# Performance work log

Measured on AMD Instinct MI355X. Metric: run time of the kernel, lower is better.

The kernel has to match this reference:

```python
import jax, jax.numpy as jnp
import numpy as np

C = 256; G = 8; GC = C // G; K = 3; PAD = 1; DIL = 1; STRIDE = 1
P = K * K
BN_EPS = 1e-5; LN_EPS = 1e-5


def setup_inputs() -> dict:
    key = jax.random.key(0)
    ks = jax.random.split(key, 8)
    def rn(k, shape, scale=0.02):
        return jax.random.normal(k, shape, jnp.float32) * scale
    B, H, W = 8, 56, 56
    return dict(
        x=jax.random.normal(ks[0], (B, C, H, W), jnp.float32),
        w_in=rn(ks[1], (C, C)), b_in=jnp.zeros((C,), jnp.float32),
        dw_w=rn(ks[2], (C, 1, K, K)), dw_b=jnp.zeros((C,), jnp.float32),
        ln_g=jnp.ones((C,), jnp.float32), ln_b=jnp.zeros((C,), jnp.float32),
        w_off=rn(ks[3], (C, G * P * 2)), b_off=jnp.zeros((G * P * 2,), jnp.float32),
        w_mask=rn(ks[4], (C, G * P)), b_mask=jnp.zeros((G * P,), jnp.float32),
        w_out=rn(ks[5], (C, C)), b_out=jnp.zeros((C,), jnp.float32),
        bn_g=jnp.ones((C,), jnp.float32), bn_b=jnp.zeros((C,), jnp.float32),
        bn_mean=jnp.zeros((C,), jnp.float32),
        bn_var=jnp.ones((C,), jnp.float32),
    )


def _forward(x, w_in, b_in, dw_w, dw_b, ln_g, ln_b, w_off, b_off,
             w_mask, b_mask, w_out, b_out, bn_g, bn_b, bn_mean, bn_var):
    B, _, H, W = x.shape
    x_nhwc = jnp.transpose(x, (0, 2, 3, 1))                    # [B,H,W,C]
    v = x_nhwc @ w_in + b_in                                   # input_proj

    # offset/mask branch: depthwise conv (NCHW) + LayerNorm (channels_last) + GELU
    f = jax.lax.conv_general_dilated(
        x, dw_w, (1, 1), [(PAD, PAD), (PAD, PAD)],
        feature_group_count=C,
        dimension_numbers=('NCHW', 'OIHW', 'NCHW')) + dw_b[None, :, None, None]
    f = jnp.transpose(f, (0, 2, 3, 1))                         # [B,H,W,C]
    mu = f.mean(-1, keepdims=True)
    var = f.var(-1, keepdims=True)
    f = (f - mu) * jax.lax.rsqrt(var + LN_EPS) * ln_g + ln_b
    f = jax.nn.gelu(f, approximate=False)

    offset = (f @ w_off + b_off).reshape(B, H, W, G, P, 2)     # (x, y) pairs
    mask = jax.nn.softmax((f @ w_mask + b_mask).reshape(B, H, W, G, P), axis=-1)

    # zero-pad projected features (dcnv3_core_pytorch pads before sampling)
    vp = jnp.pad(v, ((0, 0), (PAD, PAD), (PAD, PAD), (0, 0)))
    Hin, Win = H + 2 * PAD, W + 2 * PAD

    # reference points + kernel dilation grid, normalized to padded extent
    base = (DIL * (K - 1)) // 2 + 0.5
    ref_y = (base + jnp.arange(H, dtype=jnp.float32) * STRIDE) / Hin   # [H]
    ref_x = (base + jnp.arange(W, dtype=jnp.float32) * STRIDE) / Win   # [W]
    kx = jnp.arange(K, dtype=jnp.float32) * DIL - (DIL * (K - 1)) // 2
    gx, gy = jnp.meshgrid(kx, kx, indexing='ij')               # torch meshgrid order
    grid_x = gx.reshape(-1) / Win                              # [P]
    grid_y = gy.reshape(-1) / Hin

    loc_x = ref_x[None, None, :, None, None] + grid_x[None, None, None, None, :] + offset[..., 0] / Win
    loc_y = ref_y[None, :, None, None, None] + grid_y[None, None, None, None, :] + offset[..., 1] / Hin
    # grid_sample(align_corners=False) pixel coords: p = loc * size - 0.5
    px = loc_x * Win - 0.5                                     # [B,H,W,G,P]
    py = loc_y * Hin - 0.5

    x0 = jnp.floor(px); y0 = jnp.floor(py)
    wx = px - x0; wy = py - y0
    x0i = x0.astype(jnp.int32); y0i = y0.astype(jnp.int32)
    x1i = x0i + 1; y1i = y0i + 1

    def valid(i, lim):
        return ((i >= 0) & (i < lim)).astype(v.dtype)
    vx0, vx1 = valid(x0i, Win), valid(x1i, Win)
    vy0, vy1 = valid(y0i, Hin), valid(y1i, Hin)
    x0c = jnp.clip(x0i, 0, Win - 1); x1c = jnp.clip(x1i, 0, Win - 1)
    y0c = jnp.clip(y0i, 0, Hin - 1); y1c = jnp.clip(y1i, 0, Hin - 1)

    vg = vp.reshape(B, Hin * Win, G, GC).transpose(0, 2, 1, 3).reshape(B * G, Hin * Win, GC)
    L = H * W

    def regroup(a):  # [B,H,W,G,P] -> [B*G, L*P]
        return a.reshape(B, L, G, P).transpose(0, 2, 1, 3).reshape(B * G, L * P)

    def gather(yc, xc):
        idx = regroup(yc * Win + xc)
        return jnp.take_along_axis(vg, idx[:, :, None], axis=1)   # [B*G, L*P, GC]

    sampled = (gather(y0c, x0c) * regroup((1 - wx) * (1 - wy) * vx0 * vy0)[:, :, None]
             + gather(y0c, x1c) * regroup(wx * (1 - wy) * vx1 * vy0)[:, :, None]
             + gather(y1c, x0c) * regroup((1 - wx) * wy * vx0 * vy1)[:, :, None]
             + gather(y1c, x1c) * regroup(wx * wy * vx1 * vy1)[:, :, None])

    m = mask.reshape(B, L, G, P).transpose(0, 2, 1, 3)             # [B,G,L,P]
    out = (sampled.reshape(B, G, L, P, GC) * m[..., None]).sum(3)  # [B,G,L,GC]
    out = out.transpose(0, 2, 1, 3).reshape(B, H, W, C)

    out = out @ w_out + b_out                                  # output_proj
    y = jnp.transpose(out, (0, 3, 1, 2))                       # NCHW
    y = (y - bn_mean[None, :, None, None]) * jax.lax.rsqrt(bn_var + BN_EPS)[None, :, None, None] \
        * bn_g[None, :, None, None] + bn_b[None, :, None, None]
    return y * jax.nn.sigmoid(y)                               # SiLU


def reference(x, w_in, b_in, dw_w, dw_b, ln_g, ln_b, w_off, b_off,
              w_mask, b_mask, w_out, b_out, bn_g, bn_b, bn_mean, bn_var):
    return _forward(x, w_in, b_in, dw_w, dw_b, ln_g, ln_b, w_off, b_off,
                    w_mask, b_mask, w_out, b_out, bn_g, bn_b, bn_mean, bn_var)
```

## Files before the change

kernel.cpp:

```cpp
#include <hip/hip_runtime.h>
#include <math.h>

#define BATCH 8
#define CH    256
#define HDIM  56
#define WDIM  56
#define HW    (HDIM*WDIM)
#define MTOT  (BATCH*HW)
#define GRP   8
#define GC    32
#define NP    9
#define NOFF  (GRP*NP*2)
#define NMSK  (GRP*NP)
#define NTOT  (NOFF+NMSK)
#define POSB  4
#define DWBLK (MTOT/POSB)
#define XTBLK (49*4*8)
#define NBLKG ((MTOT/64)*2)

typedef float f32x4 __attribute__((ext_vector_type(4)));
typedef short s16x8 __attribute__((ext_vector_type(8)));

__device__ inline void split2(float a, float b, unsigned int& hp, unsigned int& lp)
{
    const unsigned int ua = __float_as_uint(a), ub = __float_as_uint(b);
    hp = (ub & 0xffff0000u) | (ua >> 16);
    const float ha = __uint_as_float(ua & 0xffff0000u);
    const float hb = __uint_as_float(ub & 0xffff0000u);
    const unsigned int la = __float_as_uint(a - ha), lb = __float_as_uint(b - hb);
    lp = (lb & 0xffff0000u) | (la >> 16);
}

__device__ __forceinline__ void gld_lds16(const unsigned short* g, unsigned short* l)
{
    __builtin_amdgcn_global_load_lds(
        (const __attribute__((address_space(1))) unsigned int*)g,
        (__attribute__((address_space(3))) unsigned int*)l, 16, 0, 0);
}

__device__ __forceinline__ void gemm64x128_body(
    const unsigned short* __restrict__ ahi,
    const unsigned short* __restrict__ alo,
    const unsigned short* __restrict__ whi,
    const unsigned short* __restrict__ wlo,
    unsigned short* sAh, unsigned short* sAl,
    unsigned short* sBh, unsigned short* sBl,
    int m0, int n0g, int t, f32x4 (&acc)[4][2])
{
    const int lane = t & 63, wv4 = t >> 6;
    const int wm = wv4 >> 1;
    const int wn = wv4 & 1;
    const int fm = lane & 15, q = lane >> 4;

    const int arow0 = t >> 2;
    const int asl0  = (t & 3) ^ ((arow0 >> 1) & 3);
    const int albase0 = wv4 * 512;
    int brow[2], bsl[2], blbase[2];
    #pragma unroll
    for (int i = 0; i < 2; ++i) {
        const int u = i * 256 + t;
        brow[i] = u >> 2;
        bsl[i] = (u & 3) ^ ((brow[i] >> 1) & 3);
        blbase[i] = i * 2048 + wv4 * 512;
    }

    for (int kk = 0; kk < 8; ++kk) {
        const int k0 = kk * 32;
        {
            const size_t ga = (size_t)(m0 + arow0) * CH + k0 + asl0 * 8;
            gld_lds16(ahi + ga, sAh + albase0);
            gld_lds16(alo + ga, sAl + albase0);
        }
        #pragma unroll
        for (int i = 0; i < 2; ++i) {
            const size_t gb = (size_t)(n0g + brow[i]) * CH + k0 + bsl[i] * 8;
            gld_lds16(whi + gb, sBh + blbase[i]);
            gld_lds16(wlo + gb, sBl + blbase[i]);
        }
        __syncthreads();

        s16x8 ah[2], al[2], wh[4], wl[4];
        #pragma unroll
        for (int i = 0; i < 2; ++i) {
            const int ar = wm * 32 + i * 16 + fm;
            const int as = (q ^ ((ar >> 1) & 3)) * 8;
            ah[i] = *(const s16x8*)&sAh[ar * 32 + as];
            al[i] = *(const s16x8*)&sAl[ar * 32 + as];
        }
        #pragma unroll
        for (int i = 0; i < 4; ++i) {
            const int br = wn * 64 + i * 16 + fm;
            const int bs = (q ^ ((br >> 1) & 3)) * 8;
            wh[i] = *(const s16x8*)&sBh[br * 32 + bs];
            wl[i] = *(const s16x8*)&sBl[br * 32 + bs];
        }
        #pragma unroll
        for (int nt = 0; nt < 4; ++nt)
            #pragma unroll
            for (int mt = 0; mt < 2; ++mt) {
                acc[nt][mt] = __builtin_amdgcn_mfma_f32_16x16x32_bf16(wh[nt], ah[mt], acc[nt][mt], 0, 0, 0);
                acc[nt][mt] = __builtin_amdgcn_mfma_f32_16x16x32_bf16(wh[nt], al[mt], acc[nt][mt], 0, 0, 0);
                acc[nt][mt] = __builtin_amdgcn_mfma_f32_16x16x32_bf16(wl[nt], ah[mt], acc[nt][mt], 0, 0, 0);
            }
        __syncthreads();
    }
}

__device__ __forceinline__ void dw_body(
    const unsigned short* __restrict__ xhi,
    const unsigned short* __restrict__ xlo,
    const float* __restrict__ dw_w,
    const float* __restrict__ dw_b,
    const float* __restrict__ ln_g,
    const float* __restrict__ ln_b,
    unsigned short* __restrict__ fh,
    unsigned short* __restrict__ fl,
    float* wt, float* lbias, float* lgam, float* lbet,
    int bid, int t)
{
    {
        const float* wp = dw_w + t * NP;
        #pragma unroll
        for (int p = 0; p < NP; ++p) wt[p * CH + t] = wp[p];
        lbias[t] = dw_b[t]; lgam[t] = ln_g[t]; lbet[t] = ln_b[t];
    }
    __syncthreads();

    const int per = DWBLK / 8;
    const int sw  = (bid & 7) * per + (bid >> 3);
    const int q   = t >> 6, lane = t & 63;
    const int n   = sw * POSB + q;
    const int b   = n / HW;
    const int hw  = n % HW;
    const int h   = hw / WDIM, w = hw % WDIM;
    const int c4  = lane * 4;
    const size_t base = (size_t)b * HW * CH + c4;

    float ax = 0.0f, ay = 0.0f, az = 0.0f, aw = 0.0f;
    #pragma unroll
    for (int p = 0; p < NP; ++p) {
        const int hh = h + p / 3 - 1;
        const int ww = w + p % 3 - 1;
        if ((unsigned)hh >= (unsigned)HDIM || (unsigned)ww >= (unsigned)WDIM)
            continue;
        const size_t idx = base + (size_t)(hh * WDIM + ww) * CH;
        const ushort4 uh = *(const ushort4*)(xhi + idx);
        const ushort4 ul = *(const ushort4*)(xlo + idx);
        const float4 wv = *(const float4*)&wt[p * CH + c4];
        ax = fmaf(__uint_as_float((unsigned)uh.x << 16), wv.x,
             fmaf(__uint_as_float((unsigned)ul.x << 16), wv.x, ax));
        ay = fmaf(__uint_as_float((unsigned)uh.y << 16), wv.y,
             fmaf(__uint_as_float((unsigned)ul.y << 16), wv.y, ay));
        az = fmaf(__uint_as_float((unsigned)uh.z << 16), wv.z,
             fmaf(__uint_as_float((unsigned)ul.z << 16), wv.z, az));
        aw = fmaf(__uint_as_float((unsigned)uh.w << 16), wv.w,
             fmaf(__uint_as_float((unsigned)ul.w << 16), wv.w, aw));
    }
    {
        const float4 b4 = *(const float4*)&lbias[c4];
        ax += b4.x; ay += b4.y; az += b4.z; aw += b4.w;
    }

    float s1 = ax + ay + az + aw;
    float s2 = ax*ax + ay*ay + az*az + aw*aw;
    #pragma unroll
    for (int off = 32; off > 0; off >>= 1) {
        s1 += __shfl_xor(s1, off);
        s2 += __shfl_xor(s2, off);
    }
    const float mean = s1 * (1.0f / 256.0f);
    const float rstd = rsqrtf(s2 * (1.0f / 256.0f) - mean * mean + 1e-5f);

    const float4 g4 = *(const float4*)&lgam[c4];
    const float4 e4 = *(const float4*)&lbet[c4];
    const float x0 = (ax - mean) * rstd * g4.x + e4.x;
    const float x1 = (ay - mean) * rstd * g4.y + e4.y;
    const float x2 = (az - mean) * rstd * g4.z + e4.z;
    const float x3 = (aw - mean) * rstd * g4.w + e4.w;
    const float o0 = 0.5f * x0 * (1.0f + erff(x0 * 0.70710678118654752f));
    const float o1 = 0.5f * x1 * (1.0f + erff(x1 * 0.70710678118654752f));
    const float o2 = 0.5f * x2 * (1.0f + erff(x2 * 0.70710678118654752f));
    const float o3 = 0.5f * x3 * (1.0f + erff(x3 * 0.70710678118654752f));

    unsigned int hp0, lp0, hp1, lp1;
    split2(o0, o1, hp0, lp0);
    split2(o2, o3, hp1, lp1);
    *(uint2*)&fh[(size_t)n * CH + c4] = make_uint2(hp0, hp1);
    *(uint2*)&fl[(size_t)n * CH + c4] = make_uint2(lp0, lp1);
}

__global__ __launch_bounds__(256)
void prep_kernel(const float* __restrict__ x,
                 unsigned short* __restrict__ xt_hi,
                 unsigned short* __restrict__ xt_lo,
                 const float* __restrict__ w_out,
                 unsigned short* __restrict__ wt_hi,
                 unsigned short* __restrict__ wt_lo,
                 const float* __restrict__ w_in,
                 unsigned short* __restrict__ wt3_hi,
                 unsigned short* __restrict__ wt3_lo,
                 const float* __restrict__ w_off,
                 const float* __restrict__ w_mask,
                 const float* __restrict__ b_off,
                 const float* __restrict__ b_mask,
                 unsigned short* __restrict__ wt2_hi,
                 unsigned short* __restrict__ wt2_lo,
                 float* __restrict__ bcat)
{
    __shared__ float lds[64][68];
    const int bid = blockIdx.x;
    const int t = threadIdx.x;

    if (bid < XTBLK) {
        const int hw0 = (bid % 49) * 64;
        const int k0  = ((bid / 49) % 4) * 64;
        const int b   = bid / 196;
        #pragma unroll
        for (int p = 0; p < 4; ++p) {
            const int kr = (t >> 4) + p * 16;
            const int hc = (t & 15) * 4;
            *(float4*)&lds[kr][hc] =
                *(const float4*)(x + ((size_t)b * CH + k0 + kr) * HW + hw0 + hc);
        }
        __syncthreads();
        const int ml = t >> 2;
        const int kc = (t & 3) * 16;
        unsigned int hbuf[8], lbuf[8];
        #pragma unroll
        for (int j = 0; j < 16; j += 2)
            split2(lds[kc + j][ml], lds[kc + j + 1][ml], hbuf[j >> 1], lbuf[j >> 1]);
        const size_t row = (size_t)(b * HW + hw0 + ml) * CH + k0 + kc;
        *(uint4*)&xt_hi[row]     = *(uint4*)&hbuf[0];
        *(uint4*)&xt_hi[row + 8] = *(uint4*)&hbuf[4];
        *(uint4*)&xt_lo[row]     = *(uint4*)&lbuf[0];
        *(uint4*)&xt_lo[row + 8] = *(uint4*)&lbuf[4];
    } else if (bid < XTBLK + 32) {
        const int u = bid - XTBLK;
        const float* w = (u < 16) ? w_out : w_in;
        unsigned short* hi = (u < 16) ? wt_hi : wt3_hi;
        unsigned short* lo = (u < 16) ? wt_lo : wt3_lo;
        const int uu = u & 15;
        const int kt = (uu & 3) * 64, nt = (uu >> 2) * 64;
        #pragma unroll
        for (int p = 0; p < 4; ++p) {
            const int kr = (t >> 4) + p * 16, nc = (t & 15) * 4;
            *(float4*)&lds[kr][nc] = *(const float4*)(w + (size_t)(kt + kr) * CH + nt + nc);
        }
        __syncthreads();
        const int nl = t >> 2, kc = (t & 3) * 16;
        #pragma unroll
        for (int j = 0; j < 16; j += 2) {
            const float f0 = lds[kc + j][nl], f1 = lds[kc + j + 1][nl];
            unsigned int hp, lp;
            split2(f0, f1, hp, lp);
            *(unsigned int*)&hi[(size_t)(nt + nl) * CH + kt + kc + j] = hp;
            *(unsigned int*)&lo[(size_t)(nt + nl) * CH + kt + kc + j] = lp;
        }
    } else {
        const int u = bid - XTBLK - 32;
        const int n = t;
        if (u == 0) {
            bcat[n] = (n < NOFF) ? b_off[n] : ((n < NTOT) ? b_mask[n - NOFF] : 0.0f);
        }
        const int k0 = u * 16;
        #pragma unroll
        for (int j = 0; j < 16; j += 2) {
            const int k = k0 + j;
            float f0 = 0.0f, f1 = 0.0f;
            if (n < NOFF) {
                f0 = w_off[(size_t)k * NOFF + n];
                f1 = w_off[(size_t)(k + 1) * NOFF + n];
            } else if (n < NTOT) {
                f0 = w_mask[(size_t)k * NMSK + (n - NOFF)];
                f1 = w_mask[(size_t)(k + 1) * NMSK + (n - NOFF)];
            }
            unsigned int hp, lp;
            split2(f0, f1, hp, lp);
            *(unsigned int*)&wt2_hi[(size_t)n * CH + k] = hp;
            *(unsigned int*)&wt2_lo[(size_t)n * CH + k] = lp;
        }
    }
}

__global__ __launch_bounds__(256)
void dw_and_gemm_v(const unsigned short* __restrict__ xhi,
                   const unsigned short* __restrict__ xlo,
                   const float* __restrict__ dw_w,
                   const float* __restrict__ dw_b,
                   const float* __restrict__ ln_g,
                   const float* __restrict__ ln_b,
                   unsigned short* __restrict__ fh,
                   unsigned short* __restrict__ fl,
                   const unsigned short* __restrict__ whi,
                   const unsigned short* __restrict__ wlo,
                   const float* __restrict__ bias,
                   float* __restrict__ v)
{
    __shared__ alignas(16) char smem[24576];
    const int bid = blockIdx.x;
    const int t = threadIdx.x;

    if (bid < DWBLK) {
        float* wt    = (float*)smem;
        float* lbias = (float*)(smem + NP * CH * 4);
        float* lgam  = lbias + CH;
        float* lbet  = lgam + CH;
        dw_body(xhi, xlo, dw_w, dw_b, ln_g, ln_b, fh, fl,
                wt, lbias, lgam, lbet, bid, t);
    } else {
        unsigned short* sAh = (unsigned short*)smem;
        unsigned short* sAl = sAh + 64 * 32;
        unsigned short* sBh = sAl + 64 * 32;
        unsigned short* sBl = sBh + 128 * 32;
        const int lbid = bid - DWBLK;
        const int sw = (lbid & 7) * (NBLKG / 8) + (lbid >> 3);
        const int m0  = (sw >> 1) * 64;
        const int n0g = (sw & 1) * 128;
        const int lane = t & 63, wv4 = t >> 6;
        const int wm = wv4 >> 1, wn = wv4 & 1;
        const int fm = lane & 15, q = lane >> 4;

        f32x4 acc[4][2];
        const f32x4 zero = {0.0f, 0.0f, 0.0f, 0.0f};
        #pragma unroll
        for (int i = 0; i < 4; ++i)
            #pragma unroll
            for (int j = 0; j < 2; ++j) acc[i][j] = zero;

        gemm64x128_body(xhi, xlo, whi, wlo, sAh, sAl, sBh, sBl, m0, n0g, t, acc);

        #pragma unroll
        for (int nt = 0; nt < 4; ++nt) {
            const int n = n0g + wn*64 + nt*16 + q*4;
            const float4 b4 = *(const float4*)&bias[n];
            #pragma unroll
            for (int mt = 0; mt < 2; ++mt) {
                const int mm = m0 + wm*32 + mt*16 + fm;
                f32x4 o = acc[nt][mt];
                o[0] += b4.x; o[1] += b4.y; o[2] += b4.z; o[3] += b4.w;
                *(f32x4*)&v[(size_t)mm * CH + n] = o;
            }
        }
    }
}

__global__ __launch_bounds__(256)
void gemm_omb(const unsigned short* __restrict__ ahi,
              const unsigned short* __restrict__ alo,
              const unsigned short* __restrict__ whi,
              const unsigned short* __restrict__ wlo,
              const float* __restrict__ bias,
              float* __restrict__ omb)
{
    __shared__ unsigned short sAh[64*32], sAl[64*32], sBh[128*32], sBl[128*32];

    const int sw = (blockIdx.x & 7) * (NBLKG / 8) + (blockIdx.x >> 3);
    const int m0  = (sw >> 1) * 64;
    const int n0g = (sw & 1) * 128;
    const int t = threadIdx.x;
    const int lane = t & 63, wv4 = t >> 6;
    const int wm = wv4 >> 1, wn = wv4 & 1;
    const int fm = lane & 15, q = lane >> 4;

    f32x4 acc[4][2];
    const f32x4 zero = {0.0f, 0.0f, 0.0f, 0.0f};
    #pragma unroll
    for (int i = 0; i < 4; ++i)
        #pragma unroll
        for (int j = 0; j < 2; ++j) acc[i][j] = zero;

    gemm64x128_body(ahi, alo, whi, wlo, sAh, sAl, sBh, sBl, m0, n0g, t, acc);

    #pragma unroll
    for (int nt = 0; nt < 4; ++nt) {
        const int n = n0g + wn*64 + nt*16 + q*4;
        const float4 b4 = *(const float4*)&bias[n];
        #pragma unroll
        for (int mt = 0; mt < 2; ++mt) {
            const int mm = m0 + wm*32 + mt*16 + fm;
            f32x4 o = acc[nt][mt];
            o[0] += b4.x; o[1] += b4.y; o[2] += b4.z; o[3] += b4.w;
            *(f32x4*)&omb[(size_t)mm * CH + n] = o;
        }
    }
}

__global__ __launch_bounds__(256)
void gemm_out_64x128(const unsigned short* __restrict__ ahi,
                     const unsigned short* __restrict__ alo,
                     const unsigned short* __restrict__ whi,
                     const unsigned short* __restrict__ wlo,
                     const float* __restrict__ bias,
                     const float* __restrict__ bn_g,
                     const float* __restrict__ bn_b,
                     const float* __restrict__ bn_mean,
                     const float* __restrict__ bn_var,
                     float* __restrict__ y)
{
    __shared__ unsigned short sAh[64*32], sAl[64*32], sBh[128*32], sBl[128*32];

    const int sw = (blockIdx.x & 7) * (NBLKG / 8) + (blockIdx.x >> 3);
    const int m0  = (sw >> 1) * 64;
    const int n0g = (sw & 1) * 128;
    const int t = threadIdx.x;
    const int lane = t & 63, wv4 = t >> 6;
    const int wm = wv4 >> 1, wn = wv4 & 1;
    const int fm = lane & 15, q = lane >> 4;

    f32x4 acc[4][2];
    const f32x4 zero = {0.0f, 0.0f, 0.0f, 0.0f};
    #pragma unroll
    for (int i = 0; i < 4; ++i)
        #pragma unroll
        for (int j = 0; j < 2; ++j) acc[i][j] = zero;

    gemm64x128_body(ahi, alo, whi, wlo, sAh, sAl, sBh, sBl, m0, n0g, t, acc);

    #pragma unroll
    for (int nt = 0; nt < 4; ++nt) {
        #pragma unroll
        for (int r = 0; r < 4; ++r) {
            const int n = n0g + wn*64 + nt*16 + q*4 + r;
            const float sc = bn_g[n] * rsqrtf(bn_var[n] + 1e-5f);
            const float sb = bn_b[n] - bn_mean[n] * sc;
            const float bs = bias[n];
            #pragma unroll
            for (int mt = 0; mt < 2; ++mt) {
                const int mm = m0 + wm*32 + mt*16 + fm;
                const int bimg = mm / HW, hw = mm % HW;
                float val = (acc[nt][mt][r] + bs) * sc + sb;
                y[(size_t)bimg * CH * HW + (size_t)n * HW + hw] = val / (1.0f + expf(-val));
            }
        }
    }
}

__global__ __launch_bounds__(256)
void sample_kernel_omb_split(const float* __restrict__ v,
                             const float* __restrict__ omb,
                             unsigned short* __restrict__ sh,
                             unsigned short* __restrict__ sl)
{
    __shared__ alignas(16) float loff[POSB][NOFF];
    __shared__ alignas(16) float lmsk[POSB][NMSK];
    __shared__ alignas(16) float wtab[POSB][GRP*NP][4];
    __shared__ alignas(16) int   itab[POSB][GRP*NP][4];

    const int per  = DWBLK / 8;
    const int bid  = blockIdx.x;
    const int sw   = (bid % 8) * per + (bid / 8);
    const int n0 = sw * POSB;
    const int t = threadIdx.x;

    if (t < POSB * (NOFF/4)) {
        const int q = t / (NOFF/4), r = t % (NOFF/4);
        *(float4*)&loff[q][r*4] = *(const float4*)&omb[(size_t)(n0+q)*CH + r*4];
    } else if (t < POSB * (NOFF/4) + POSB * (NMSK/4)) {
        const int u = t - POSB * (NOFF/4);
        const int q = u / (NMSK/4), r = u % (NMSK/4);
        *(float4*)&lmsk[q][r*4] = *(const float4*)&omb[(size_t)(n0+q)*CH + NOFF + r*4];
    }
    __syncthreads();

    if (t < POSB * GRP) {
        const int q = t >> 3, g = t & 7;
        float* mm = &lmsk[q][g * NP];
        float mx = -1e30f;
        #pragma unroll
        for (int p = 0; p < NP; ++p) mx = fmaxf(mx, mm[p]);
        float sum = 0.0f;
        #pragma unroll
        for (int p = 0; p < NP; ++p) { const float e = __expf(mm[p] - mx); mm[p] = e; sum += e; }
        const float inv = 1.0f / sum;
        #pragma unroll
        for (int p = 0; p < NP; ++p) mm[p] *= inv;
    }
    __syncthreads();

    for (int u = t; u < POSB * GRP * NP; u += 256) {
        const int q = u / (GRP*NP), j = u % (GRP*NP);
        const int g = j / NP, p = j % NP;
        const int n = n0 + q;
        const int hw = n % HW;
        const int h = hw / WDIM, w = hw % WDIM;
        const float ox = loff[q][g*18 + p*2 + 0];
        const float oy = loff[q][g*18 + p*2 + 1];
        const float m  = lmsk[q][g*NP + p];
        const float px = (float)(w + p/3) + ox;
        const float py = (float)(h + p%3) + oy;
        const float fx = floorf(px), fy = floorf(py);
        const float wx = px - fx, wy = py - fy;
        const int x0 = (int)fx, y0 = (int)fy;
        const int x1 = x0 + 1, y1 = y0 + 1;
        const float vx0 = (x0 >= 1 && x0 < 57) ? 1.0f : 0.0f;
        const float vx1 = (x1 >= 1 && x1 < 57) ? 1.0f : 0.0f;
        const float vy0 = (y0 >= 1 && y0 < 57) ? 1.0f : 0.0f;
        const float vy1 = (y1 >= 1 && y1 < 57) ? 1.0f : 0.0f;
        const int x0c = min(max(x0, 1), 56), x1c = min(max(x1, 1), 56);
        const int y0c = min(max(y0, 1), 56), y1c = min(max(y1, 1), 56);
        wtab[q][j][0] = m * (1.0f-wx) * (1.0f-wy) * vx0 * vy0;
        wtab[q][j][1] = m * wx        * (1.0f-wy) * vx1 * vy0;
        wtab[q][j][2] = m * (1.0f-wx) * wy        * vx0 * vy1;
        wtab[q][j][3] = m * wx        * wy        * vx1 * vy1;
        itab[q][j][0] = ((y0c-1)*WDIM + (x0c-1)) * CH;
        itab[q][j][1] = ((y0c-1)*WDIM + (x1c-1)) * CH;
        itab[q][j][2] = ((y1c-1)*WDIM + (x0c-1)) * CH;
        itab[q][j][3] = ((y1c-1)*WDIM + (x1c-1)) * CH;
    }
    __syncthreads();

    const int q = t >> 6, lane = t & 63;
    const int n = n0 + q;
    const int b = n / HW;
    const int g = lane >> 3;
    const float* vb = v + (size_t)b*HW*CH + lane*4;
    float4 acc = {0.0f, 0.0f, 0.0f, 0.0f};
    #pragma unroll
    for (int p = 0; p < NP; ++p) {
        const int j = g*NP + p;
        const float4 wv = *(const float4*)&wtab[q][j][0];
        const int4  iv = *(const int4*)&itab[q][j][0];
        const float4 c0 = *(const float4*)(vb + iv.x);
        const float4 c1 = *(const float4*)(vb + iv.y);
        const float4 c2 = *(const float4*)(vb + iv.z);
        const float4 c3 = *(const float4*)(vb + iv.w);
        acc.x += wv.x*c0.x + wv.y*c1.x + wv.z*c2.x + wv.w*c3.x;
        acc.y += wv.x*c0.y + wv.y*c1.y + wv.z*c2.y + wv.w*c3.y;
        acc.z += wv.x*c0.z + wv.y*c1.z + wv.z*c2.z + wv.w*c3.z;
        acc.w += wv.x*c0.w + wv.y*c1.w + wv.z*c2.w + wv.w*c3.w;
    }
    unsigned int hp0, lp0, hp1, lp1;
    split2(acc.x, acc.y, hp0, lp0);
    split2(acc.z, acc.w, hp1, lp1);
    *(uint2*)&sh[(size_t)n*CH + lane*4] = make_uint2(hp0, hp1);
    *(uint2*)&sl[(size_t)n*CH + lane*4] = make_uint2(lp0, lp1);
}

__global__ __launch_bounds__(256)
void xt_split_kernel(const float* __restrict__ x,
                     unsigned short* __restrict__ hi,
                     unsigned short* __restrict__ lo)
{
    __shared__ float lds[64][68];
    const int hw0 = blockIdx.x * 64;
    const int k0  = blockIdx.y * 64;
    const int b   = blockIdx.z;
    const int t = threadIdx.x;
    #pragma unroll
    for (int p = 0; p < 4; ++p) {
        const int kr = (t >> 4) + p * 16;
        const int hc = (t & 15) * 4;
        *(float4*)&lds[kr][hc] =
            *(const float4*)(x + ((size_t)b * CH + k0 + kr) * HW + hw0 + hc);
    }
    __syncthreads();
    const int ml = t >> 2;
    const int kc = (t & 3) * 16;
    unsigned int hbuf[8], lbuf[8];
    #pragma unroll
    for (int j = 0; j < 16; j += 2)
        split2(lds[kc + j][ml], lds[kc + j + 1][ml], hbuf[j >> 1], lbuf[j >> 1]);
    const size_t row = (size_t)(b * HW + hw0 + ml) * CH + k0 + kc;
    *(uint4*)&hi[row]     = *(uint4*)&hbuf[0];
    *(uint4*)&hi[row + 8] = *(uint4*)&hbuf[4];
    *(uint4*)&lo[row]     = *(uint4*)&lbuf[0];
    *(uint4*)&lo[row + 8] = *(uint4*)&lbuf[4];
}

__global__ __launch_bounds__(256)
void wt_split_kernel(const float* __restrict__ w,
                     unsigned short* __restrict__ hi,
                     unsigned short* __restrict__ lo)
{
    __shared__ float lds[64][68];
    const int kt = blockIdx.x * 64, nt = blockIdx.y * 64;
    const int t = threadIdx.x;
    #pragma unroll
    for (int p = 0; p < 4; ++p) {
        const int kr = (t >> 4) + p * 16, nc = (t & 15) * 4;
        *(float4*)&lds[kr][nc] = *(const float4*)(w + (size_t)(kt + kr) * CH + nt + nc);
    }
    __syncthreads();
    const int nl = t >> 2, kc = (t & 3) * 16;
    #pragma unroll
    for (int j = 0; j < 16; j += 2) {
        const float f0 = lds[kc + j][nl], f1 = lds[kc + j + 1][nl];
        unsigned int hp, lp;
        split2(f0, f1, hp, lp);
        *(unsigned int*)&hi[(size_t)(nt + nl) * CH + kt + kc + j] = hp;
        *(unsigned int*)&lo[(size_t)(nt + nl) * CH + kt + kc + j] = lp;
    }
}

__global__ __launch_bounds__(256)
void wt2_split_kernel(const float* __restrict__ w_off,
                      const float* __restrict__ w_mask,
                      const float* __restrict__ b_off,
                      const float* __restrict__ b_mask,
                      unsigned short* __restrict__ hi,
                      unsigned short* __restrict__ lo,
                      float* __restrict__ bcat)
{
    const int n = threadIdx.x;
    if (blockIdx.x == 0) {
        bcat[n] = (n < NOFF) ? b_off[n] : ((n < NTOT) ? b_mask[n - NOFF] : 0.0f);
    }
    const int k0 = blockIdx.x * 16;
    #pragma unroll
    for (int j = 0; j < 16; j += 2) {
        const int k = k0 + j;
        float f0 = 0.0f, f1 = 0.0f;
        if (n < NOFF) {
            f0 = w_off[(size_t)k * NOFF + n];
            f1 = w_off[(size_t)(k + 1) * NOFF + n];
        } else if (n < NTOT) {
            f0 = w_mask[(size_t)k * NMSK + (n - NOFF)];
            f1 = w_mask[(size_t)(k + 1) * NMSK + (n - NOFF)];
        }
        unsigned int hp, lp;
        split2(f0, f1, hp, lp);
        *(unsigned int*)&hi[(size_t)n * CH + k] = hp;
        *(unsigned int*)&lo[(size_t)n * CH + k] = lp;
    }
}

__global__ __launch_bounds__(256)
void gemm_in_mfma(const unsigned short* __restrict__ xhi,
                  const unsigned short* __restrict__ xlo,
                  const unsigned short* __restrict__ whi,
                  const unsigned short* __restrict__ wlo,
                  const float* __restrict__ bias,
                  float* __restrict__ v)
{
    const int m0 = blockIdx.x * 256;
    const int n0 = blockIdx.y * 64;
    const int t = threadIdx.x;
    const int lane = t & 63, wv = t >> 6;
    const int mblk = m0 + wv * 64;
    const int fm = lane & 15;
    const int q  = lane >> 4;

    f32x4 acc[4][4];
    const f32x4 zero = {0.0f, 0.0f, 0.0f, 0.0f};
    #pragma unroll
    for (int i = 0; i < 4; ++i)
        #pragma unroll
        for (int j = 0; j < 4; ++j) acc[i][j] = zero;

    const unsigned short *xrh[4], *xrl[4], *wrh[4], *wrl[4];
    #pragma unroll
    for (int mt = 0; mt < 4; ++mt) {
        xrh[mt] = xhi + (size_t)(mblk + mt*16 + fm) * CH + q * 8;
        xrl[mt] = xlo + (size_t)(mblk + mt*16 + fm) * CH + q * 8;
    }
    #pragma unroll
    for (int nt = 0; nt < 4; ++nt) {
        wrh[nt] = whi + (size_t)(n0 + nt*16 + fm) * CH + q * 8;
        wrl[nt] = wlo + (size_t)(n0 + nt*16 + fm) * CH + q * 8;
    }

    for (int k0 = 0; k0 < CH; k0 += 32) {
        s16x8 wh[4], wl[4], ah[4], al[4];
        #pragma unroll
        for (int nt = 0; nt < 4; ++nt) {
            wh[nt] = *(const s16x8*)(wrh[nt] + k0);
            wl[nt] = *(const s16x8*)(wrl[nt] + k0);
        }
        #pragma unroll
        for (int mt = 0; mt < 4; ++mt) {
            ah[mt] = *(const s16x8*)(xrh[mt] + k0);
            al[mt] = *(const s16x8*)(xrl[mt] + k0);
        }
        #pragma unroll
        for (int nt = 0; nt < 4; ++nt)
            #pragma unroll
            for (int mt = 0; mt < 4; ++mt) {
                acc[nt][mt] = __builtin_amdgcn_mfma_f32_16x16x32_bf16(wh[nt], ah[mt], acc[nt][mt], 0, 0, 0);
                acc[nt][mt] = __builtin_amdgcn_mfma_f32_16x16x32_bf16(wh[nt], al[mt], acc[nt][mt], 0, 0, 0);
                acc[nt][mt] = __builtin_amdgcn_mfma_f32_16x16x32_bf16(wl[nt], ah[mt], acc[nt][mt], 0, 0, 0);
            }
    }

    #pragma unroll
    for (int nt = 0; nt < 4; ++nt) {
        const float4 b4 = *(const float4*)&bias[n0 + nt*16 + q*4];
        #pragma unroll
        for (int mt = 0; mt < 4; ++mt) {
            f32x4 o = acc[nt][mt];
            o[0] += b4.x; o[1] += b4.y; o[2] += b4.z; o[3] += b4.w;
            *(f32x4*)&v[(size_t)(mblk + mt*16 + fm) * CH + n0 + nt*16 + q*4] = o;
        }
    }
}

__global__ __launch_bounds__(256)
void dw_ln_gelu_nhwc_split(const unsigned short* __restrict__ xhi,
                           const unsigned short* __restrict__ xlo,
                           const float* __restrict__ dw_w,
                           const float* __restrict__ dw_b,
                           const float* __restrict__ ln_g,
                           const float* __restrict__ ln_b,
                           unsigned short* __restrict__ fh,
                           unsigned short* __restrict__ fl)
{
    __shared__ float wt[NP][CH];
    __shared__ float lbias[CH], lgam[CH], lbet[CH];
    const int t = threadIdx.x;
    {
        const float* wp = dw_w + t * NP;
        #pragma unroll
        for (int p = 0; p < NP; ++p) wt[p][t] = wp[p];
        lbias[t] = dw_b[t]; lgam[t] = ln_g[t]; lbet[t] = ln_b[t];
    }
    __syncthreads();

    const int per  = DWBLK / 8;
    const int bid  = blockIdx.x;
    const int sw   = (bid & 7) * per + (bid >> 3);
    const int q    = t >> 6, lane = t & 63;
    const int n    = sw * POSB + q;
    const int b    = n / HW;
    const int hw   = n % HW;
    const int h    = hw / WDIM, w = hw % WDIM;
    const int c4   = lane * 4;
    const size_t base = (size_t)b * HW * CH + c4;

    float ax = 0.0f, ay = 0.0f, az = 0.0f, aw = 0.0f;
    #pragma unroll
    for (int p = 0; p < NP; ++p) {
        const int hh = h + p / 3 - 1;
        const int ww = w + p % 3 - 1;
        if ((unsigned)hh >= (unsigned)HDIM || (unsigned)ww >= (unsigned)WDIM)
            continue;
        const size_t idx = base + (size_t)(hh * WDIM + ww) * CH;
        const ushort4 uh = *(const ushort4*)(xhi + idx);
        const ushort4 ul = *(const ushort4*)(xlo + idx);
        const float4 wv = *(const float4*)&wt[p][c4];
        ax = fmaf(__uint_as_float((unsigned)uh.x << 16), wv.x,
             fmaf(__uint_as_float((unsigned)ul.x << 16), wv.x, ax));
        ay = fmaf(__uint_as_float((unsigned)uh.y << 16), wv.y,
             fmaf(__uint_as_float((unsigned)ul.y << 16), wv.y, ay));
        az = fmaf(__uint_as_float((unsigned)uh.z << 16), wv.z,
             fmaf(__uint_as_float((unsigned)ul.z << 16), wv.z, az));
        aw = fmaf(__uint_as_float((unsigned)uh.w << 16), wv.w,
             fmaf(__uint_as_float((unsigned)ul.w << 16), wv.w, aw));
    }
    {
        const float4 b4 = *(const float4*)&lbias[c4];
        ax += b4.x; ay += b4.y; az += b4.z; aw += b4.w;
    }
    float s1 = ax + ay + az + aw;
    float s2 = ax*ax + ay*ay + az*az + aw*aw;
    #pragma unroll
    for (int off = 32; off > 0; off >>= 1) {
        s1 += __shfl_xor(s1, off);
        s2 += __shfl_xor(s2, off);
    }
    const float mean = s1 * (1.0f / 256.0f);
    const float rstd = rsqrtf(s2 * (1.0f / 256.0f) - mean * mean + 1e-5f);
    const float4 g4 = *(const float4*)&lgam[c4];
    const float4 e4 = *(const float4*)&lbet[c4];
    const float x0 = (ax - mean) * rstd * g4.x + e4.x;
    const float x1 = (ay - mean) * rstd * g4.y + e4.y;
    const float x2 = (az - mean) * rstd * g4.z + e4.z;
    const float x3 = (aw - mean) * rstd * g4.w + e4.w;
    const float o0 = 0.5f * x0 * (1.0f + erff(x0 * 0.70710678118654752f));
    const float o1 = 0.5f * x1 * (1.0f + erff(x1 * 0.70710678118654752f));
    const float o2 = 0.5f * x2 * (1.0f + erff(x2 * 0.70710678118654752f));
    const float o3 = 0.5f * x3 * (1.0f + erff(x3 * 0.70710678118654752f));
    unsigned int hp0, lp0, hp1, lp1;
    split2(o0, o1, hp0, lp0);
    split2(o2, o3, hp1, lp1);
    *(uint2*)&fh[(size_t)n * CH + c4] = make_uint2(hp0, hp1);
    *(uint2*)&fl[(size_t)n * CH + c4] = make_uint2(lp0, lp1);
}

__global__ __launch_bounds__(256)
void gemm_out_bf16(const unsigned short* __restrict__ shp,
                   const unsigned short* __restrict__ slp,
                   const unsigned short* __restrict__ whi,
                   const unsigned short* __restrict__ wlo,
                   const float* __restrict__ bias,
                   const float* __restrict__ bn_g,
                   const float* __restrict__ bn_b,
                   const float* __restrict__ bn_mean,
                   const float* __restrict__ bn_var,
                   float* __restrict__ y)
{
    const int m0 = blockIdx.x * 256;
    const int n0 = blockIdx.y * 64;
    const int t = threadIdx.x;
    const int lane = t & 63, wv = t >> 6;
    const int mblk = m0 + wv * 64;
    const int fm = lane & 15;
    const int q  = lane >> 4;

    f32x4 acc[4][4];
    const f32x4 zero = {0.0f, 0.0f, 0.0f, 0.0f};
    #pragma unroll
    for (int i = 0; i < 4; ++i)
        #pragma unroll
        for (int j = 0; j < 4; ++j) acc[i][j] = zero;

    const unsigned short *xrh[4], *xrl[4], *wrh[4], *wrl[4];
    #pragma unroll
    for (int mt = 0; mt < 4; ++mt) {
        xrh[mt] = shp + (size_t)(mblk + mt*16 + fm) * CH + q * 8;
        xrl[mt] = slp + (size_t)(mblk + mt*16 + fm) * CH + q * 8;
    }
    #pragma unroll
    for (int nt = 0; nt < 4; ++nt) {
        wrh[nt] = whi + (size_t)(n0 + nt*16 + fm) * CH + q * 8;
        wrl[nt] = wlo + (size_t)(n0 + nt*16 + fm) * CH + q * 8;
    }

    for (int k0 = 0; k0 < CH; k0 += 32) {
        s16x8 wh[4], wl[4], ah[4], al[4];
        #pragma unroll
        for (int nt = 0; nt < 4; ++nt) {
            wh[nt] = *(const s16x8*)(wrh[nt] + k0);
            wl[nt] = *(const s16x8*)(wrl[nt] + k0);
        }
        #pragma unroll
        for (int mt = 0; mt < 4; ++mt) {
            ah[mt] = *(const s16x8*)(xrh[mt] + k0);
            al[mt] = *(const s16x8*)(xrl[mt] + k0);
        }
        #pragma unroll
        for (int nt = 0; nt < 4; ++nt)
            #pragma unroll
            for (int mt = 0; mt < 4; ++mt) {
                acc[nt][mt] = __builtin_amdgcn_mfma_f32_16x16x32_bf16(wh[nt], ah[mt], acc[nt][mt], 0, 0, 0);
                acc[nt][mt] = __builtin_amdgcn_mfma_f32_16x16x32_bf16(wh[nt], al[mt], acc[nt][mt], 0, 0, 0);
                acc[nt][mt] = __builtin_amdgcn_mfma_f32_16x16x32_bf16(wl[nt], ah[mt], acc[nt][mt], 0, 0, 0);
            }
    }

    #pragma unroll
    for (int nt = 0; nt < 4; ++nt) {
        #pragma unroll
        for (int r = 0; r < 4; ++r) {
            const int n = n0 + nt*16 + q*4 + r;
            const float sc = bn_g[n] * rsqrtf(bn_var[n] + 1e-5f);
            const float sb = bn_b[n] - bn_mean[n] * sc;
            const float bs = bias[n];
            #pragma unroll
            for (int mt = 0; mt < 4; ++mt) {
                const int mm = mblk + mt*16;
                const size_t base = (size_t)(mm / HW) * CH * HW + (mm % HW);
                float val = (acc[nt][mt][r] + bs) * sc + sb;
                y[base + (size_t)n * HW + fm] = val / (1.0f + expf(-val));
            }
        }
    }
}

extern "C" void kernel_launch(void* const* d_in, const int* in_sizes, int n_in,
                              void* d_out, int out_size, void* d_ws, size_t ws_size,
                              hipStream_t stream) {
    const float* x      = (const float*)d_in[0];
    const float* w_in   = (const float*)d_in[1];
    const float* b_in   = (const float*)d_in[2];
    const float* dw_w   = (const float*)d_in[3];
    const float* dw_b   = (const float*)d_in[4];
    const float* ln_g   = (const float*)d_in[5];
    const float* ln_b   = (const float*)d_in[6];
    const float* w_off  = (const float*)d_in[7];
    const float* b_off  = (const float*)d_in[8];
    const float* w_mask = (const float*)d_in[9];
    const float* b_mask = (const float*)d_in[10];
    const float* w_out  = (const float*)d_in[11];
    const float* b_out  = (const float*)d_in[12];
    const float* bn_g   = (const float*)d_in[13];
    const float* bn_b   = (const float*)d_in[14];
    const float* bn_mean= (const float*)d_in[15];
    const float* bn_var = (const float*)d_in[16];
    float* out = (float*)d_out;

    const size_t SZ = (size_t)MTOT * CH;
    const size_t need_new =
        4 * SZ * sizeof(float)
        + 6 * (size_t)CH * CH * sizeof(unsigned short)
        + CH * sizeof(float);

    if (ws_size >= need_new) {
        float* ws = (float*)d_ws;
        float* v    = ws;
        unsigned short* xt_hi = (unsigned short*)(v + SZ);
        unsigned short* xt_lo = xt_hi + SZ;
        unsigned short* fh    = xt_lo + SZ;
        unsigned short* fl    = fh + SZ;
        float* omb  = (float*)(fl + SZ);
        unsigned short* wt_hi  = (unsigned short*)(omb + SZ);
        unsigned short* wt_lo  = wt_hi + CH * CH;
        unsigned short* wt2_hi = wt_lo + CH * CH;
        unsigned short* wt2_lo = wt2_hi + CH * CH;
        unsigned short* wt3_hi = wt2_lo + CH * CH;
        unsigned short* wt3_lo = wt3_hi + CH * CH;
        float* bcat = (float*)(wt3_lo + CH * CH);
        unsigned short* sh = xt_hi;
        unsigned short* sl = xt_lo;

        prep_kernel<<<dim3(XTBLK + 48), dim3(256), 0, stream>>>(
            x, xt_hi, xt_lo, w_out, wt_hi, wt_lo, w_in, wt3_hi, wt3_lo,
            w_off, w_mask, b_off, b_mask, wt2_hi, wt2_lo, bcat);
        dw_and_gemm_v<<<dim3(DWBLK + NBLKG), dim3(256), 0, stream>>>(
            xt_hi, xt_lo, dw_w, dw_b, ln_g, ln_b, fh, fl,
            wt3_hi, wt3_lo, b_in, v);
        gemm_omb<<<dim3(NBLKG), dim3(256), 0, stream>>>(
            fh, fl, wt2_hi, wt2_lo, bcat, omb);
        sample_kernel_omb_split<<<dim3(DWBLK), dim3(256), 0, stream>>>(v, omb, sh, sl);
        gemm_out_64x128<<<dim3(NBLKG), dim3(256), 0, stream>>>(
            sh, sl, wt_hi, wt_lo, b_out, bn_g, bn_b, bn_mean, bn_var, out);
    } else {
        float* ws = (float*)d_ws;
        float* v    = ws;
        unsigned short* xt_hi = (unsigned short*)(v + SZ);
        unsigned short* xt_lo = xt_hi + SZ;
        unsigned short* fh    = xt_lo + SZ;
        unsigned short* fl    = fh + SZ;
        float* omb  = (float*)(fl + SZ);
        unsigned short* wt_hi  = (unsigned short*)(omb + SZ);
        unsigned short* wt_lo  = wt_hi + CH * CH;
        unsigned short* wt2_hi = wt_lo + CH * CH;
        unsigned short* wt2_lo = wt2_hi + CH * CH;
        unsigned short* wt3_hi = wt2_lo + CH * CH;
        unsigned short* wt3_lo = wt3_hi + CH * CH;
        float* bcat = (float*)(wt3_lo + CH * CH);
        unsigned short* sh = xt_hi;
        unsigned short* sl = xt_lo;

        wt_split_kernel<<<dim3(4, 4), dim3(256), 0, stream>>>(w_out, wt_hi, wt_lo);
        wt_split_kernel<<<dim3(4, 4), dim3(256), 0, stream>>>(w_in, wt3_hi, wt3_lo);
        wt2_split_kernel<<<dim3(16), dim3(256), 0, stream>>>(
            w_off, w_mask, b_off, b_mask, wt2_hi, wt2_lo, bcat);
        xt_split_kernel<<<dim3(HW/64, CH/64, BATCH), dim3(256), 0, stream>>>(x, xt_hi, xt_lo);
        gemm_in_mfma<<<dim3(MTOT/256, CH/64), dim3(256), 0, stream>>>(
            xt_hi, xt_lo, wt3_hi, wt3_lo, b_in, v);
        dw_ln_gelu_nhwc_split<<<dim3(DWBLK), dim3(256), 0, stream>>>(
            xt_hi, xt_lo, dw_w, dw_b, ln_g, ln_b, fh, fl);
        gemm_in_mfma<<<dim3(MTOT/256, CH/64), dim3(256), 0, stream>>>(
            fh, fl, wt2_hi, wt2_lo, bcat, omb);
        sample_kernel_omb_split<<<dim3(DWBLK), dim3(256), 0, stream>>>(v, omb, sh, sl);
        gemm_out_bf16<<<dim3(MTOT/256, CH/64), dim3(256), 0, stream>>>(
            sh, sl, wt_hi, wt_lo, b_out, bn_g, bn_b, bn_mean, bn_var, out);
    }
}
```

Measured before the change: 229.3 us.

## Regroup input-proj GEMM with offset/mask GEMM instead of depthwise kernel

Moves the input-projection GEMM (v = x·w_in) out of the combined depthwise+GEMM launch and into a dual GEMM launch alongside the offset/mask GEMM. The depthwise LN/GELU kernel now runs alone. The two GEMMs have identical shapes, so they share one homogeneous grid instead of mixing memory-bound depthwise blocks with MFMA blocks, which had different shared-memory and register needs. The trade-off is that the input-projection GEMM no longer overlaps with the depthwise stage.

```diff
diff --git a/kernel.cpp b/kernel.cpp
--- a/kernel.cpp
+++ b/kernel.cpp
@@ -106,89 +106,6 @@
     }
 }
 
-__device__ __forceinline__ void dw_body(
-    const unsigned short* __restrict__ xhi,
-    const unsigned short* __restrict__ xlo,
-    const float* __restrict__ dw_w,
-    const float* __restrict__ dw_b,
-    const float* __restrict__ ln_g,
-    const float* __restrict__ ln_b,
-    unsigned short* __restrict__ fh,
-    unsigned short* __restrict__ fl,
-    float* wt, float* lbias, float* lgam, float* lbet,
-    int bid, int t)
-{
-    {
-        const float* wp = dw_w + t * NP;
-        #pragma unroll
-        for (int p = 0; p < NP; ++p) wt[p * CH + t] = wp[p];
-        lbias[t] = dw_b[t]; lgam[t] = ln_g[t]; lbet[t] = ln_b[t];
-    }
-    __syncthreads();
-
-    const int per = DWBLK / 8;
-    const int sw  = (bid & 7) * per + (bid >> 3);
-    const int q   = t >> 6, lane = t & 63;
-    const int n   = sw * POSB + q;
-    const int b   = n / HW;
-    const int hw  = n % HW;
-    const int h   = hw / WDIM, w = hw % WDIM;
-    const int c4  = lane * 4;
-    const size_t base = (size_t)b * HW * CH + c4;
-
-    float ax = 0.0f, ay = 0.0f, az = 0.0f, aw = 0.0f;
-    #pragma unroll
-    for (int p = 0; p < NP; ++p) {
-        const int hh = h + p / 3 - 1;
-        const int ww = w + p % 3 - 1;
-        if ((unsigned)hh >= (unsigned)HDIM || (unsigned)ww >= (unsigned)WDIM)
-            continue;
-        const size_t idx = base + (size_t)(hh * WDIM + ww) * CH;
-        const ushort4 uh = *(const ushort4*)(xhi + idx);
-        const ushort4 ul = *(const ushort4*)(xlo + idx);
-        const float4 wv = *(const float4*)&wt[p * CH + c4];
-        ax = fmaf(__uint_as_float((unsigned)uh.x << 16), wv.x,
-             fmaf(__uint_as_float((unsigned)ul.x << 16), wv.x, ax));
-        ay = fmaf(__uint_as_float((unsigned)uh.y << 16), wv.y,
-             fmaf(__uint_as_float((unsigned)ul.y << 16), wv.y, ay));
-        az = fmaf(__uint_as_float((unsigned)uh.z << 16), wv.z,
-             fmaf(__uint_as_float((unsigned)ul.z << 16), wv.z, az));
-        aw = fmaf(__uint_as_float((unsigned)uh.w << 16), wv.w,
-             fmaf(__uint_as_float((unsigned)ul.w << 16), wv.w, aw));
-    }
-    {
-        const float4 b4 = *(const float4*)&lbias[c4];
-        ax += b4.x; ay += b4.y; az += b4.z; aw += b4.w;
-    }
-
-    float s1 = ax + ay + az + aw;
-    float s2 = ax*ax + ay*ay + az*az + aw*aw;
-    #pragma unroll
-    for (int off = 32; off > 0; off >>= 1) {
-        s1 += __shfl_xor(s1, off);
-        s2 += __shfl_xor(s2, off);
-    }
-    const float mean = s1 * (1.0f / 256.0f);
-    const float rstd = rsqrtf(s2 * (1.0f / 256.0f) - mean * mean + 1e-5f);
-
-    const float4 g4 = *(const float4*)&lgam[c4];
-    const float4 e4 = *(const float4*)&lbet[c4];
-    const float x0 = (ax - mean) * rstd * g4.x + e4.x;
-    const float x1 = (ay - mean) * rstd * g4.y + e4.y;
-    const float x2 = (az - mean) * rstd * g4.z + e4.z;
-    const float x3 = (aw - mean) * rstd * g4.w + e4.w;
-    const float o0 = 0.5f * x0 * (1.0f + erff(x0 * 0.70710678118654752f));
-    const float o1 = 0.5f * x1 * (1.0f + erff(x1 * 0.70710678118654752f));
-    const float o2 = 0.5f * x2 * (1.0f + erff(x2 * 0.70710678118654752f));
-    const float o3 = 0.5f * x3 * (1.0f + erff(x3 * 0.70710678118654752f));
-
-    unsigned int hp0, lp0, hp1, lp1;
-    split2(o0, o1, hp0, lp0);
-    split2(o2, o3, hp1, lp1);
-    *(uint2*)&fh[(size_t)n * CH + c4] = make_uint2(hp0, hp1);
-    *(uint2*)&fl[(size_t)n * CH + c4] = make_uint2(lp0, lp1);
-}
-
 __global__ __launch_bounds__(256)
 void prep_kernel(const float* __restrict__ x,
                  unsigned short* __restrict__ xt_hi,
@@ -283,78 +200,113 @@
 }
 
 __global__ __launch_bounds__(256)
-void dw_and_gemm_v(const unsigned short* __restrict__ xhi,
-                   const unsigned short* __restrict__ xlo,
-                   const float* __restrict__ dw_w,
-                   const float* __restrict__ dw_b,
-                   const float* __restrict__ ln_g,
-                   const float* __restrict__ ln_b,
-                   unsigned short* __restrict__ fh,
-                   unsigned short* __restrict__ fl,
-                   const unsigned short* __restrict__ whi,
-                   const unsigned short* __restrict__ wlo,
-                   const float* __restrict__ bias,
-                   float* __restrict__ v)
-{
-    __shared__ alignas(16) char smem[24576];
-    const int bid = blockIdx.x;
+void dw_ln_gelu_nhwc_split(const unsigned short* __restrict__ xhi,
+                           const unsigned short* __restrict__ xlo,
+                           const float* __restrict__ dw_w,
+                           const float* __restrict__ dw_b,
+                           const float* __restrict__ ln_g,
+                           const float* __restrict__ ln_b,
+                           unsigned short* __restrict__ fh,
+                           unsigned short* __restrict__ fl)
+{
+    __shared__ float wt[NP][CH];
+    __shared__ float lbias[CH], lgam[CH], lbet[CH];
     const int t = threadIdx.x;
-
-    if (bid < DWBLK) {
-        float* wt    = (float*)smem;
-        float* lbias = (float*)(smem + NP * CH * 4);
-        float* lgam  = lbias + CH;
-        float* lbet  = lgam + CH;
-        dw_body(xhi, xlo, dw_w, dw_b, ln_g, ln_b, fh, fl,
-                wt, lbias, lgam, lbet, bid, t);
-    } else {
-        unsigned short* sAh = (unsigned short*)smem;
-        unsigned short* sAl = sAh + 64 * 32;
-        unsigned short* sBh = sAl + 64 * 32;
-        unsigned short* sBl = sBh + 128 * 32;
-        const int lbid = bid - DWBLK;
-        const int sw = (lbid & 7) * (NBLKG / 8) + (lbid >> 3);
-        const int m0  = (sw >> 1) * 64;
-        const int n0g = (sw & 1) * 128;
-        const int lane = t & 63, wv4 = t >> 6;
-        const int wm = wv4 >> 1, wn = wv4 & 1;
-        const int fm = lane & 15, q = lane >> 4;
-
-        f32x4 acc[4][2];
-        const f32x4 zero = {0.0f, 0.0f, 0.0f, 0.0f};
-        #pragma unroll
-        for (int i = 0; i < 4; ++i)
-            #pragma unroll
-            for (int j = 0; j < 2; ++j) acc[i][j] = zero;
-
-        gemm64x128_body(xhi, xlo, whi, wlo, sAh, sAl, sBh, sBl, m0, n0g, t, acc);
-
-        #pragma unroll
-        for (int nt = 0; nt < 4; ++nt) {
-            const int n = n0g + wn*64 + nt*16 + q*4;
-            const float4 b4 = *(const float4*)&bias[n];
-            #pragma unroll
-            for (int mt = 0; mt < 2; ++mt) {
-                const int mm = m0 + wm*32 + mt*16 + fm;
-                f32x4 o = acc[nt][mt];
-                o[0] += b4.x; o[1] += b4.y; o[2] += b4.z; o[3] += b4.w;
-                *(f32x4*)&v[(size_t)mm * CH + n] = o;
-            }
-        }
-    }
-}
-
-__global__ __launch_bounds__(256)
-void gemm_omb(const unsigned short* __restrict__ ahi,
-              const unsigned short* __restrict__ alo,
-              const unsigned short* __restrict__ whi,
-              const unsigned short* __restrict__ wlo,
-              const float* __restrict__ bias,
-              float* __restrict__ omb)
+    {
+        const float* wp = dw_w + t * NP;
+        #pragma unroll
+        for (int p = 0; p < NP; ++p) wt[p][t] = wp[p];
+        lbias[t] = dw_b[t]; lgam[t] = ln_g[t]; lbet[t] = ln_b[t];
+    }
+    __syncthreads();
+
+    const int per  = DWBLK / 8;
+    const int bid  = blockIdx.x;
+    const int sw   = (bid & 7) * per + (bid >> 3);
+    const int q    = t >> 6, lane = t & 63;
+    const int n    = sw * POSB + q;
+    const int b    = n / HW;
+    const int hw   = n % HW;
+    const int h    = hw / WDIM, w = hw % WDIM;
+    const int c4   = lane * 4;
+    const size_t base = (size_t)b * HW * CH + c4;
+
+    float ax = 0.0f, ay = 0.0f, az = 0.0f, aw = 0.0f;
+    #pragma unroll
+    for (int p = 0; p < NP; ++p) {
+        const int hh = h + p / 3 - 1;
+        const int ww = w + p % 3 - 1;
+        if ((unsigned)hh >= (unsigned)HDIM || (unsigned)ww >= (unsigned)WDIM)
+            continue;
+        const size_t idx = base + (size_t)(hh * WDIM + ww) * CH;
+        const ushort4 uh = *(const ushort4*)(xhi + idx);
+        const ushort4 ul = *(const ushort4*)(xlo + idx);
+        const float4 wv = *(const float4*)&wt[p][c4];
+        ax = fmaf(__uint_as_float((unsigned)uh.x << 16), wv.x,
+             fmaf(__uint_as_float((unsigned)ul.x << 16), wv.x, ax));
+        ay = fmaf(__uint_as_float((unsigned)uh.y << 16), wv.y,
+             fmaf(__uint_as_float((unsigned)ul.y << 16), wv.y, ay));
+        az = fmaf(__uint_as_float((unsigned)uh.z << 16), wv.z,
+             fmaf(__uint_as_float((unsigned)ul.z << 16), wv.z, az));
+        aw = fmaf(__uint_as_float((unsigned)uh.w << 16), wv.w,
+             fmaf(__uint_as_float((unsigned)ul.w << 16), wv.w, aw));
+    }
+    {
+        const float4 b4 = *(const float4*)&lbias[c4];
+        ax += b4.x; ay += b4.y; az += b4.z; aw += b4.w;
+    }
+    float s1 = ax + ay + az + aw;
+    float s2 = ax*ax + ay*ay + az*az + aw*aw;
+    #pragma unroll
+    for (int off = 32; off > 0; off >>= 1) {
+        s1 += __shfl_xor(s1, off);
+        s2 += __shfl_xor(s2, off);
+    }
+    const float mean = s1 * (1.0f / 256.0f);
+    const float rstd = rsqrtf(s2 * (1.0f / 256.0f) - mean * mean + 1e-5f);
+    const float4 g4 = *(const float4*)&lgam[c4];
+    const float4 e4 = *(const float4*)&lbet[c4];
+    const float x0 = (ax - mean) * rstd * g4.x + e4.x;
+    const float x1 = (ay - mean) * rstd * g4.y + e4.y;
+    const float x2 = (az - mean) * rstd * g4.z + e4.z;
+    const float x3 = (aw - mean) * rstd * g4.w + e4.w;
+    const float o0 = 0.5f * x0 * (1.0f + erff(x0 * 0.70710678118654752f));
+    const float o1 = 0.5f * x1 * (1.0f + erff(x1 * 0.70710678118654752f));
+    const float o2 = 0.5f * x2 * (1.0f + erff(x2 * 0.70710678118654752f));
+    const float o3 = 0.5f * x3 * (1.0f + erff(x3 * 0.70710678118654752f));
+    unsigned int hp0, lp0, hp1, lp1;
+    split2(o0, o1, hp0, lp0);
+    split2(o2, o3, hp1, lp1);
+    *(uint2*)&fh[(size_t)n * CH + c4] = make_uint2(hp0, hp1);
+    *(uint2*)&fl[(size_t)n * CH + c4] = make_uint2(lp0, lp1);
+}
+
+__global__ __launch_bounds__(256)
+void gemm_dual64(const unsigned short* __restrict__ ahi1,
+                 const unsigned short* __restrict__ alo1,
+                 const unsigned short* __restrict__ whi1,
+                 const unsigned short* __restrict__ wlo1,
+                 const float* __restrict__ bias1,
+                 float* __restrict__ out1,
+                 const unsigned short* __restrict__ ahi2,
+                 const unsigned short* __restrict__ alo2,
+                 const unsigned short* __restrict__ whi2,
+                 const unsigned short* __restrict__ wlo2,
+                 const float* __restrict__ bias2,
+                 float* __restrict__ out2)
 {
     __shared__ unsigned short sAh[64*32], sAl[64*32], sBh[128*32], sBl[128*32];
 
-    const int sw = (blockIdx.x & 7) * (NBLKG / 8) + (blockIdx.x >> 3);
+    const int half = blockIdx.x >= NBLKG;
+    const int lbid = blockIdx.x - (half ? NBLKG : 0);
+    const unsigned short* ahi = half ? ahi2 : ahi1;
+    const unsigned short* alo = half ? alo2 : alo1;
+    const unsigned short* whi = half ? whi2 : whi1;
+    const unsigned short* wlo = half ? wlo2 : wlo1;
+    const float* bias = half ? bias2 : bias1;
+    float* out = half ? out2 : out1;
+
+    const int sw = (lbid & 7) * (NBLKG / 8) + (lbid >> 3);
     const int m0  = (sw >> 1) * 64;
     const int n0g = (sw & 1) * 128;
     const int t = threadIdx.x;
@@ -380,7 +332,7 @@
             const int mm = m0 + wm*32 + mt*16 + fm;
             f32x4 o = acc[nt][mt];
             o[0] += b4.x; o[1] += b4.y; o[2] += b4.z; o[3] += b4.w;
-            *(f32x4*)&omb[(size_t)mm * CH + n] = o;
+            *(f32x4*)&out[(size_t)mm * CH + n] = o;
         }
     }
 }
@@ -694,88 +646,6 @@
 }
 
 __global__ __launch_bounds__(256)
-void dw_ln_gelu_nhwc_split(const unsigned short* __restrict__ xhi,
-                           const unsigned short* __restrict__ xlo,
-                           const float* __restrict__ dw_w,
-                           const float* __restrict__ dw_b,
-                           const float* __restrict__ ln_g,
-                           const float* __restrict__ ln_b,
-                           unsigned short* __restrict__ fh,
-                           unsigned short* __restrict__ fl)
-{
-    __shared__ float wt[NP][CH];
-    __shared__ float lbias[CH], lgam[CH], lbet[CH];
-    const int t = threadIdx.x;
-    {
-        const float* wp = dw_w + t * NP;
-        #pragma unroll
-        for (int p = 0; p < NP; ++p) wt[p][t] = wp[p];
-        lbias[t] = dw_b[t]; lgam[t] = ln_g[t]; lbet[t] = ln_b[t];
-    }
-    __syncthreads();
-
-    const int per  = DWBLK / 8;
-    const int bid  = blockIdx.x;
-    const int sw   = (bid & 7) * per + (bid >> 3);
-    const int q    = t >> 6, lane = t & 63;
-    const int n    = sw * POSB + q;
-    const int b    = n / HW;
-    const int hw   = n % HW;
-    const int h    = hw / WDIM, w = hw % WDIM;
-    const int c4   = lane * 4;
-    const size_t base = (size_t)b * HW * CH + c4;
-
-    float ax = 0.0f, ay = 0.0f, az = 0.0f, aw = 0.0f;
-    #pragma unroll
-    for (int p = 0; p < NP; ++p) {
-        const int hh = h + p / 3 - 1;
-        const int ww = w + p % 3 - 1;
-        if ((unsigned)hh >= (unsigned)HDIM || (unsigned)ww >= (unsigned)WDIM)
-            continue;
-        const size_t idx = base + (size_t)(hh * WDIM + ww) * CH;
-        const ushort4 uh = *(const ushort4*)(xhi + idx);
-        const ushort4 ul = *(const ushort4*)(xlo + idx);
-        const float4 wv = *(const float4*)&wt[p][c4];
-        ax = fmaf(__uint_as_float((unsigned)uh.x << 16), wv.x,
-             fmaf(__uint_as_float((unsigned)ul.x << 16), wv.x, ax));
-        ay = fmaf(__uint_as_float((unsigned)uh.y << 16), wv.y,
-             fmaf(__uint_as_float((unsigned)ul.y << 16), wv.y, ay));
-        az = fmaf(__uint_as_float((unsigned)uh.z << 16), wv.z,
-             fmaf(__uint_as_float((unsigned)ul.z << 16), wv.z, az));
-        aw = fmaf(__uint_as_float((unsigned)uh.w << 16), wv.w,
-             fmaf(__uint_as_float((unsigned)ul.w << 16), wv.w, aw));
-    }
-    {
-        const float4 b4 = *(const float4*)&lbias[c4];
-        ax += b4.x; ay += b4.y; az += b4.z; aw += b4.w;
-    }
-    float s1 = ax + ay + az + aw;
-    float s2 = ax*ax + ay*ay + az*az + aw*aw;
-    #pragma unroll
-    for (int off = 32; off > 0; off >>= 1) {
-        s1 += __shfl_xor(s1, off);
-        s2 += __shfl_xor(s2, off);
-    }
-    const float mean = s1 * (1.0f / 256.0f);
-    const float rstd = rsqrtf(s2 * (1.0f / 256.0f) - mean * mean + 1e-5f);
-    const float4 g4 = *(const float4*)&lgam[c4];
-    const float4 e4 = *(const float4*)&lbet[c4];
-    const float x0 = (ax - mean) * rstd * g4.x + e4.x;
-    const float x1 = (ay - mean) * rstd * g4.y + e4.y;
-    const float x2 = (az - mean) * rstd * g4.z + e4.z;
-    const float x3 = (aw - mean) * rstd * g4.w + e4.w;
-    const float o0 = 0.5f * x0 * (1.0f + erff(x0 * 0.70710678118654752f));
-    const float o1 = 0.5f * x1 * (1.0f + erff(x1 * 0.70710678118654752f));
-    const float o2 = 0.5f * x2 * (1.0f + erff(x2 * 0.70710678118654752f));
-    const float o3 = 0.5f * x3 * (1.0f + erff(x3 * 0.70710678118654752f));
-    unsigned int hp0, lp0, hp1, lp1;
-    split2(o0, o1, hp0, lp0);
-    split2(o2, o3, hp1, lp1);
-    *(uint2*)&fh[(size_t)n * CH + c4] = make_uint2(hp0, hp1);
-    *(uint2*)&fl[(size_t)n * CH + c4] = make_uint2(lp0, lp1);
-}
-
-__global__ __launch_bounds__(256)
 void gemm_out_bf16(const unsigned short* __restrict__ shp,
                    const unsigned short* __restrict__ slp,
                    const unsigned short* __restrict__ whi,
@@ -904,10 +774,10 @@
         prep_kernel<<<dim3(XTBLK + 48), dim3(256), 0, stream>>>(
             x, xt_hi, xt_lo, w_out, wt_hi, wt_lo, w_in, wt3_hi, wt3_lo,
             w_off, w_mask, b_off, b_mask, wt2_hi, wt2_lo, bcat);
-        dw_and_gemm_v<<<dim3(DWBLK + NBLKG), dim3(256), 0, stream>>>(
-            xt_hi, xt_lo, dw_w, dw_b, ln_g, ln_b, fh, fl,
-            wt3_hi, wt3_lo, b_in, v);
-        gemm_omb<<<dim3(NBLKG), dim3(256), 0, stream>>>(
+        dw_ln_gelu_nhwc_split<<<dim3(DWBLK), dim3(256), 0, stream>>>(
+            xt_hi, xt_lo, dw_w, dw_b, ln_g, ln_b, fh, fl);
+        gemm_dual64<<<dim3(2 * NBLKG), dim3(256), 0, stream>>>(
+            xt_hi, xt_lo, wt3_hi, wt3_lo, b_in, v,
             fh, fl, wt2_hi, wt2_lo, bcat, omb);
         sample_kernel_omb_split<<<dim3(DWBLK), dim3(256), 0, stream>>>(v, omb, sh, sl);
         gemm_out_64x128<<<dim3(NBLKG), dim3(256), 0, stream>>>(
```

Result: faster. 224.3 us (-2.2%).
